# Kernel tuning notes

Hardware: AMD Instinct MI355X
Metric: run time of the kernel (lower is better)

## Reference

```python
import jax, jax.numpy as jnp
import numpy as np

N_NODES = 50000
N_EDGES = 800000
IN_C, HID_C, OUT_C = 256, 512, 256


def _linear_params(key, fan_in, fan_out):
    kw, kb = jax.random.split(key)
    bound = 1.0 / np.sqrt(fan_in)
    w = jax.random.uniform(kw, (fan_in, fan_out), jnp.float32, -bound, bound)
    b = jax.random.uniform(kb, (fan_out,), jnp.float32, -bound, bound)
    return w, b


def setup_inputs() -> dict:
    key = jax.random.key(0)
    ks = jax.random.split(key, 6)
    x = jax.random.normal(ks[0], (N_NODES, IN_C), jnp.float32)
    src = jax.random.randint(ks[1], (N_EDGES,), 0, N_NODES, jnp.int32)
    dst = jax.random.randint(ks[2], (N_EDGES,), 0, N_NODES, jnp.int32)
    w1, b1 = _linear_params(ks[3], IN_C, HID_C)
    w2, b2 = _linear_params(ks[4], HID_C, HID_C)
    w3, b3 = _linear_params(ks[5], HID_C, OUT_C)
    eps = jnp.zeros((), jnp.float32)  # GIN learnable eps, init 0
    return {"x": x, "src": src, "dst": dst,
            "w1": w1, "b1": b1, "eps1": eps,
            "w2": w2, "b2": b2, "eps2": eps,
            "w3": w3, "b3": b3, "eps3": eps}


def _gin_conv(h, src, dst, w, b, eps, n_nodes):
    # aggregate: (A @ h)[i] = sum over edges (src->dst==i) of h[src]
    agg = jax.ops.segment_sum(h[src], dst, num_segments=n_nodes)
    return ((1.0 + eps) * h + agg) @ w + b


def reference(x, src, dst, w1, b1, eps1, w2, b2, eps2, w3, b3, eps3):
    n = x.shape[0]
    # eval-mode forward: dropout is identity
    h = jax.nn.relu(_gin_conv(x, src, dst, w1, b1, eps1, n))
    h = jax.nn.relu(_gin_conv(h, src, dst, w2, b2, eps2, n))
    return _gin_conv(h, src, dst, w3, b3, eps3, n)
```

## Files before the change

### kernel.cpp

```cpp
#include <hip/hip_runtime.h>

#define N_NODES 50000
#define N_EDGES 800000
#define IN_C 256
#define HID_C 512
#define OUT_C 256
#define M_PAD 50048
#define NPASS 8
#define PASS_SHIFT 13

typedef unsigned short u16;
typedef unsigned int   u32;
typedef u16  u16x4 __attribute__((ext_vector_type(4)));
typedef u16  u16x8 __attribute__((ext_vector_type(8)));
typedef short s16x8 __attribute__((ext_vector_type(8)));
typedef float f32x4 __attribute__((ext_vector_type(4)));

__device__ __forceinline__ float bf2f(u16 h) {
    u32 u = ((u32)h) << 16;
    return __builtin_bit_cast(float, u);
}
__device__ __forceinline__ u16 f2bf(float f) {
    u32 u = __builtin_bit_cast(u32, f);
    u32 r = u + 0x7fffu + ((u >> 16) & 1u);
    return (u16)(r >> 16);
}
__device__ __forceinline__ void gload16(const void* g, void* l) {
    __builtin_amdgcn_global_load_lds(
        (const __attribute__((address_space(1))) u32*)g,
        (__attribute__((address_space(3))) u32*)l, 16, 0, 0);
}

__global__ void k_hist8(const int* __restrict__ src, const int* __restrict__ dst,
                        int* __restrict__ cnt8) {
    int e = blockIdx.x * 256 + threadIdx.x;
    if (e < N_EDGES) {
        int q = src[e] >> PASS_SHIFT;
        atomicAdd(&cnt8[dst[e] * NPASS + q], 1);
    }
}

__global__ void k_partial(const int* __restrict__ cnt, int* __restrict__ bsum, int total) {
    __shared__ int s[256];
    int i = blockIdx.x * 256 + threadIdx.x;
    int v = (i < total) ? cnt[i] : 0;
    s[threadIdx.x] = v; __syncthreads();
    for (int o = 128; o > 0; o >>= 1) {
        if (threadIdx.x < o) s[threadIdx.x] += s[threadIdx.x + o];
        __syncthreads();
    }
    if (threadIdx.x == 0) bsum[blockIdx.x] = s[0];
}

__global__ void k_scanb(int* __restrict__ bsum, int nb) {
    __shared__ int s[256];
    int carry = 0;
    for (int base = 0; base < nb; base += 256) {
        int i = base + threadIdx.x;
        int v = (i < nb) ? bsum[i] : 0;
        s[threadIdx.x] = v; __syncthreads();
        for (int o = 1; o < 256; o <<= 1) {
            int t = (threadIdx.x >= o) ? s[threadIdx.x - o] : 0;
            __syncthreads();
            s[threadIdx.x] += t;
            __syncthreads();
        }
        int tot = s[255];
        if (i < nb) bsum[i] = s[threadIdx.x] - v + carry;
        carry += tot;
        __syncthreads();
    }
}

__global__ void k_rowptr8(const int* __restrict__ cnt, const int* __restrict__ bsum,
                          int* __restrict__ rp, int* __restrict__ cur, int total) {
    __shared__ int s[256];
    int i = blockIdx.x * 256 + threadIdx.x;
    int v = (i < total) ? cnt[i] : 0;
    s[threadIdx.x] = v; __syncthreads();
    for (int o = 1; o < 256; o <<= 1) {
        int t = (threadIdx.x >= o) ? s[threadIdx.x - o] : 0;
        __syncthreads();
        s[threadIdx.x] += t;
        __syncthreads();
    }
    int excl = s[threadIdx.x] - v + bsum[blockIdx.x];
    if (i < total) { rp[i] = excl; cur[i] = excl; }
    if (i == total - 1) rp[total] = excl + v;
}

__global__ void k_scatter8(const int* __restrict__ src, const int* __restrict__ dst,
                           int* __restrict__ cur, int* __restrict__ col) {
    int e = blockIdx.x * 256 + threadIdx.x;
    if (e < N_EDGES) {
        int sv = src[e];
        int q = sv >> PASS_SHIFT;
        int p = atomicAdd(&cur[dst[e] * NPASS + q], 1);
        col[p] = sv;
    }
}

__global__ void k_wt(const float* __restrict__ w, u16* __restrict__ wt, int K, int N) {
    int idx = blockIdx.x * 256 + threadIdx.x;
    if (idx >= K * N) return;
    int n = idx / K, k = idx - n * K;
    wt[idx] = f2bf(w[(size_t)k * N + n]);
}

__global__ void k_x2bf(const float* __restrict__ x, u16* __restrict__ xb) {
    int i = blockIdx.x * 256 + threadIdx.x;
    if (i < N_NODES * IN_C / 4) {
        float4 v = ((const float4*)x)[i];
        u16x4 o;
        o[0] = f2bf(v.x); o[1] = f2bf(v.y); o[2] = f2bf(v.z); o[3] = f2bf(v.w);
        ((u16x4*)xb)[i] = o;
    }
}

template <int C, int EPI>
__global__ __launch_bounds__(256) void k_agg_stream(
    const u16* __restrict__ sm, const int* __restrict__ rp8,
    const int* __restrict__ col, const float* __restrict__ eps,
    const float* __restrict__ bias, void* __restrict__ out) {
    constexpr int NSLAB = C / 64;
    const int slab  = blockIdx.x & (NSLAB - 1);
    const int chunk = blockIdx.x / NSLAB;
    const int gid = threadIdx.x >> 4;
    const int ln  = threadIdx.x & 15;
    const int ch0 = slab * 64 + ln * 4;
    const int n = chunk * 16 + gid;
    if (n >= N_NODES) return;
    const float ep = 1.f + eps[0];

    const int rs = rp8[n * NPASS];
    const int re = rp8[n * NPASS + NPASS];
    float a0 = 0.f, a1 = 0.f, a2 = 0.f, a3 = 0.f;
    int e = rs;
    for (; e + 4 <= re; e += 4) {
        int s0 = col[e], s1 = col[e + 1], s2 = col[e + 2], s3 = col[e + 3];
        u16x4 v0 = *(const u16x4*)(sm + (size_t)s0 * C + ch0);
        u16x4 v1 = *(const u16x4*)(sm + (size_t)s1 * C + ch0);
        u16x4 v2 = *(const u16x4*)(sm + (size_t)s2 * C + ch0);
        u16x4 v3 = *(const u16x4*)(sm + (size_t)s3 * C + ch0);
        a0 += bf2f(v0[0]) + bf2f(v1[0]) + bf2f(v2[0]) + bf2f(v3[0]);
        a1 += bf2f(v0[1]) + bf2f(v1[1]) + bf2f(v2[1]) + bf2f(v3[1]);
        a2 += bf2f(v0[2]) + bf2f(v1[2]) + bf2f(v2[2]) + bf2f(v3[2]);
        a3 += bf2f(v0[3]) + bf2f(v1[3]) + bf2f(v2[3]) + bf2f(v3[3]);
    }
    for (; e < re; e++) {
        int s0 = col[e];
        u16x4 v0 = *(const u16x4*)(sm + (size_t)s0 * C + ch0);
        a0 += bf2f(v0[0]); a1 += bf2f(v0[1]); a2 += bf2f(v0[2]); a3 += bf2f(v0[3]);
    }

    u16x4 sv = *(const u16x4*)(sm + (size_t)n * C + ch0);
    float r0 = fmaf(ep, bf2f(sv[0]), a0);
    float r1 = fmaf(ep, bf2f(sv[1]), a1);
    float r2 = fmaf(ep, bf2f(sv[2]), a2);
    float r3 = fmaf(ep, bf2f(sv[3]), a3);
    if constexpr (EPI == 0) {
        u16x4 o;
        o[0] = f2bf(r0); o[1] = f2bf(r1); o[2] = f2bf(r2); o[3] = f2bf(r3);
        *(u16x4*)((u16*)out + (size_t)n * C + ch0) = o;
    } else {
        float4 bv = *(const float4*)(bias + ch0);
        float4 o;
        o.x = r0 + bv.x; o.y = r1 + bv.y; o.z = r2 + bv.z; o.w = r3 + bv.w;
        *(float4*)((float*)out + (size_t)n * C + ch0) = o;
    }
}

template <int K, int EPI>
__global__ __launch_bounds__(256, 2) void gemm_k(
    const u16* __restrict__ A, const u16* __restrict__ Wt,
    const float* __restrict__ bias, void* __restrict__ out,
    int N, int grid_n) {
    __shared__ u16 smem[16640];
    u16* Als = smem;
    u16* Bls = smem + 8192;
    const int tid  = threadIdx.x;
    const int wave = tid >> 6, lane = tid & 63;
    const int wm = wave >> 1, wn = wave & 1;
    const int bm = blockIdx.x / grid_n, bn = blockIdx.x % grid_n;
    const int m0 = bm * 128, n0 = bn * 128;
    const int sr = lane >> 3, sc = lane & 7;
    const int fr = lane & 15, kg = lane >> 4;

    f32x4 acc[4][4];
#pragma unroll
    for (int i = 0; i < 4; i++)
#pragma unroll
        for (int j = 0; j < 4; j++) acc[i][j] = (f32x4){0.f, 0.f, 0.f, 0.f};

    for (int kk = 0; kk < K; kk += 64) {
#pragma unroll
        for (int i = 0; i < 4; i++) {
            int rl = wave * 32 + i * 8 + sr;
            int cs = sc ^ (rl & 7);
            gload16(A  + (size_t)(m0 + rl) * K + kk + cs * 8,
                    &Als[(wave * 32 + i * 8) * 64]);
            gload16(Wt + (size_t)(n0 + rl) * K + kk + cs * 8,
                    &Bls[(wave * 32 + i * 8) * 64]);
        }
        asm volatile("s_waitcnt vmcnt(0)" ::: "memory");
        __syncthreads();

#pragma unroll
        for (int k2 = 0; k2 < 2; k2++) {
            s16x8 af[4], bfr[4];
#pragma unroll
            for (int mi = 0; mi < 4; mi++) {
                int r = wm * 64 + mi * 16 + fr;
                int c = (k2 * 4 + kg) ^ (r & 7);
                af[mi] = *(const s16x8*)&Als[r * 64 + c * 8];
            }
#pragma unroll
            for (int ni = 0; ni < 4; ni++) {
                int r = wn * 64 + ni * 16 + fr;
                int c = (k2 * 4 + kg) ^ (r & 7);
                bfr[ni] = *(const s16x8*)&Bls[r * 64 + c * 8];
            }
#pragma unroll
            for (int mi = 0; mi < 4; mi++)
#pragma unroll
                for (int ni = 0; ni < 4; ni++)
                    acc[mi][ni] = __builtin_amdgcn_mfma_f32_16x16x32_bf16(
                        af[mi], bfr[ni], acc[mi][ni], 0, 0, 0);
        }
        __syncthreads();
    }

    u16* Cls = smem;
#pragma unroll
    for (int ni = 0; ni < 4; ni++) {
        int c = wn * 64 + ni * 16 + fr;
        float bv = 0.f;
        if constexpr (EPI == 0) bv = bias[n0 + c];
#pragma unroll
        for (int mi = 0; mi < 4; mi++) {
#pragma unroll
            for (int j = 0; j < 4; j++) {
                int r = wm * 64 + mi * 16 + kg * 4 + j;
                float v = acc[mi][ni][j];
                if constexpr (EPI == 0) {
                    v += bv;
                    v = v > 0.f ? v : 0.f;
                }
                Cls[r * 130 + c] = f2bf(v);
            }
        }
    }
    __syncthreads();

    const int r2 = tid >> 1;
    const int cb = (tid & 1) * 64;
    if (m0 + r2 < N_NODES) {
        u16* orow = (u16*)out + (size_t)(m0 + r2) * N + n0 + cb;
#pragma unroll
        for (int k = 0; k < 8; k++) {
            u16x8 val = *(const u16x8*)&Cls[r2 * 130 + cb + k * 8];
            *(u16x8*)(orow + k * 8) = val;
        }
    }
}

extern "C" void kernel_launch(void* const* d_in, const int* in_sizes, int n_in,
                              void* d_out, int out_size, void* d_ws, size_t ws_size,
                              hipStream_t stream) {
    const float* x    = (const float*)d_in[0];
    const int*   src  = (const int*)d_in[1];
    const int*   dst  = (const int*)d_in[2];
    const float* w1   = (const float*)d_in[3];
    const float* b1   = (const float*)d_in[4];
    const float* eps1 = (const float*)d_in[5];
    const float* w2   = (const float*)d_in[6];
    const float* b2   = (const float*)d_in[7];
    const float* eps2 = (const float*)d_in[8];
    const float* w3   = (const float*)d_in[9];
    const float* b3   = (const float*)d_in[10];
    const float* eps3 = (const float*)d_in[11];

    char* ws = (char*)d_ws;
    size_t off = 0;
    auto take = [&](size_t bytes) {
        char* p = ws + off;
        off += (bytes + 255) & ~(size_t)255;
        return p;
    };
    const int TOT8 = N_NODES * NPASS;
    int* cnt8 = (int*)take((size_t)TOT8 * 4);
    int* rp8  = (int*)take((size_t)(TOT8 + 1) * 4);
    int* cur8 = (int*)take((size_t)TOT8 * 4);
    int* bsum = (int*)take(2048 * 4);
    int* col  = (int*)take((size_t)N_EDGES * 4);
    u16* w1t  = (u16*)take((size_t)IN_C * HID_C * 2);
    u16* w2t  = (u16*)take((size_t)HID_C * HID_C * 2);
    u16* w3t  = (u16*)take((size_t)HID_C * OUT_C * 2);
    u16* A0   = (u16*)take((size_t)M_PAD * IN_C * 2);
    u16* h1   = (u16*)take((size_t)M_PAD * HID_C * 2);
    u16* A1   = (u16*)take((size_t)M_PAD * HID_C * 2);
    u16* xb = A1;
    u16* h2 = h1;
    u16* g3 = A1;

    const int NB8 = (TOT8 + 255) / 256;
    const int NE  = (N_EDGES + 255) / 256;

    hipMemsetAsync(cnt8, 0, (size_t)TOT8 * 4, stream);
    k_hist8  <<<NE, 256, 0, stream>>>(src, dst, cnt8);
    k_partial<<<NB8, 256, 0, stream>>>(cnt8, bsum, TOT8);
    k_scanb  <<<1, 256, 0, stream>>>(bsum, NB8);
    k_rowptr8<<<NB8, 256, 0, stream>>>(cnt8, bsum, rp8, cur8, TOT8);
    k_scatter8<<<NE, 256, 0, stream>>>(src, dst, cur8, col);

    k_wt<<<(IN_C * HID_C + 255) / 256, 256, 0, stream>>>(w1, w1t, IN_C, HID_C);
    k_wt<<<(HID_C * HID_C + 255) / 256, 256, 0, stream>>>(w2, w2t, HID_C, HID_C);
    k_wt<<<(HID_C * OUT_C + 255) / 256, 256, 0, stream>>>(w3, w3t, HID_C, OUT_C);
    k_x2bf<<<(N_NODES * IN_C / 4 + 255) / 256, 256, 0, stream>>>(x, xb);

    const int NCH  = (N_NODES + 15) / 16;
    const int G512 = NCH * 8;
    const int G256 = NCH * 4;

    k_agg_stream<IN_C, 0><<<G256, 256, 0, stream>>>(xb, rp8, col, eps1, nullptr, A0);
    gemm_k<IN_C, 0><<<391 * (HID_C / 128), 256, 0, stream>>>(
        A0, w1t, b1, h1, HID_C, HID_C / 128);

    k_agg_stream<HID_C, 0><<<G512, 256, 0, stream>>>(h1, rp8, col, eps2, nullptr, A1);
    gemm_k<HID_C, 0><<<391 * (HID_C / 128), 256, 0, stream>>>(
        A1, w2t, b2, h2, HID_C, HID_C / 128);

    gemm_k<HID_C, 1><<<391 * (OUT_C / 128), 256, 0, stream>>>(
        h2, w3t, nullptr, g3, OUT_C, OUT_C / 128);
    k_agg_stream<OUT_C, 1><<<G256, 256, 0, stream>>>(g3, rp8, col, eps3, b3, (float*)d_out);
}
```

Before: 459.1 us.

## Sort nodes by degree for balanced aggregation and fuse prep kernels

Adds a counting sort of nodes by in-degree (histogram, scan, scatter) and has each aggregation thread group process nodes in that permuted order. Nodes with similar degree then share a wavefront, which is meant to cut divergence and idle lanes. The four weight-transpose and input-conversion launches are merged into one kernel to save launch overhead. The cost is three extra small kernels plus an indirection, and output rows are written in scattered rather than sequential order, which may hurt locality.

```diff
diff --git a/kernel.cpp b/kernel.cpp
--- a/kernel.cpp
+++ b/kernel.cpp
@@ -100,36 +100,83 @@
     }
 }
 
-__global__ void k_wt(const float* __restrict__ w, u16* __restrict__ wt, int K, int N) {
-    int idx = blockIdx.x * 256 + threadIdx.x;
+__global__ void k_deg(const int* __restrict__ rp8, int* __restrict__ dbin) {
+    int n = blockIdx.x * 256 + threadIdx.x;
+    if (n < N_NODES) {
+        int deg = rp8[n * NPASS + NPASS] - rp8[n * NPASS];
+        if (deg > 255) deg = 255;
+        atomicAdd(&dbin[deg], 1);
+    }
+}
+
+__global__ void k_degscan(const int* __restrict__ dbin, int* __restrict__ dcur) {
+    __shared__ int s[256];
+    int i = threadIdx.x;
+    int v = dbin[i];
+    s[i] = v; __syncthreads();
+    for (int o = 1; o < 256; o <<= 1) {
+        int t = (i >= o) ? s[i - o] : 0;
+        __syncthreads();
+        s[i] += t;
+        __syncthreads();
+    }
+    dcur[i] = s[i] - v;
+}
+
+__global__ void k_degscatter(const int* __restrict__ rp8, int* __restrict__ dcur,
+                             int* __restrict__ perm) {
+    int n = blockIdx.x * 256 + threadIdx.x;
+    if (n < N_NODES) {
+        int deg = rp8[n * NPASS + NPASS] - rp8[n * NPASS];
+        if (deg > 255) deg = 255;
+        int pos = atomicAdd(&dcur[deg], 1);
+        perm[pos] = n;
+    }
+}
+
+__device__ __forceinline__ void wt_body(const float* w, u16* wt, int K, int N, int idx) {
     if (idx >= K * N) return;
     int n = idx / K, k = idx - n * K;
     wt[idx] = f2bf(w[(size_t)k * N + n]);
 }
 
-__global__ void k_x2bf(const float* __restrict__ x, u16* __restrict__ xb) {
-    int i = blockIdx.x * 256 + threadIdx.x;
-    if (i < N_NODES * IN_C / 4) {
-        float4 v = ((const float4*)x)[i];
-        u16x4 o;
-        o[0] = f2bf(v.x); o[1] = f2bf(v.y); o[2] = f2bf(v.z); o[3] = f2bf(v.w);
-        ((u16x4*)xb)[i] = o;
+__global__ void k_prep(const float* __restrict__ w1, const float* __restrict__ w2,
+                       const float* __restrict__ w3, const float* __restrict__ x,
+                       u16* __restrict__ w1t, u16* __restrict__ w2t,
+                       u16* __restrict__ w3t, u16* __restrict__ xb) {
+    int b = blockIdx.x, t = threadIdx.x;
+    if (b < 512) {
+        wt_body(w1, w1t, IN_C, HID_C, b * 256 + t);
+    } else if (b < 1536) {
+        wt_body(w2, w2t, HID_C, HID_C, (b - 512) * 256 + t);
+    } else if (b < 2048) {
+        wt_body(w3, w3t, HID_C, OUT_C, (b - 1536) * 256 + t);
+    } else {
+        int i = (b - 2048) * 256 + t;
+        if (i < N_NODES * IN_C / 4) {
+            float4 v = ((const float4*)x)[i];
+            u16x4 o;
+            o[0] = f2bf(v.x); o[1] = f2bf(v.y); o[2] = f2bf(v.z); o[3] = f2bf(v.w);
+            ((u16x4*)xb)[i] = o;
+        }
     }
 }
 
 template <int C, int EPI>
 __global__ __launch_bounds__(256) void k_agg_stream(
     const u16* __restrict__ sm, const int* __restrict__ rp8,
-    const int* __restrict__ col, const float* __restrict__ eps,
-    const float* __restrict__ bias, void* __restrict__ out) {
+    const int* __restrict__ col, const int* __restrict__ perm,
+    const float* __restrict__ eps, const float* __restrict__ bias,
+    void* __restrict__ out) {
     constexpr int NSLAB = C / 64;
     const int slab  = blockIdx.x & (NSLAB - 1);
     const int chunk = blockIdx.x / NSLAB;
     const int gid = threadIdx.x >> 4;
     const int ln  = threadIdx.x & 15;
     const int ch0 = slab * 64 + ln * 4;
-    const int n = chunk * 16 + gid;
-    if (n >= N_NODES) return;
+    const int ni = chunk * 16 + gid;
+    if (ni >= N_NODES) return;
+    const int n = perm[ni];
     const float ep = 1.f + eps[0];
 
     const int rs = rp8[n * NPASS];
@@ -293,6 +340,9 @@
     int* cur8 = (int*)take((size_t)TOT8 * 4);
     int* bsum = (int*)take(2048 * 4);
     int* col  = (int*)take((size_t)N_EDGES * 4);
+    int* dbin = (int*)take(256 * 4);
+    int* dcur = (int*)take(256 * 4);
+    int* perm = (int*)take((size_t)N_NODES * 4);
     u16* w1t  = (u16*)take((size_t)IN_C * HID_C * 2);
     u16* w2t  = (u16*)take((size_t)HID_C * HID_C * 2);
     u16* w3t  = (u16*)take((size_t)HID_C * OUT_C * 2);
@@ -305,32 +355,38 @@
 
     const int NB8 = (TOT8 + 255) / 256;
     const int NE  = (N_EDGES + 255) / 256;
+    const int NBN = (N_NODES + 255) / 256;
 
     hipMemsetAsync(cnt8, 0, (size_t)TOT8 * 4, stream);
+    hipMemsetAsync(dbin, 0, 256 * 4, stream);
     k_hist8  <<<NE, 256, 0, stream>>>(src, dst, cnt8);
     k_partial<<<NB8, 256, 0, stream>>>(cnt8, bsum, TOT8);
     k_scanb  <<<1, 256, 0, stream>>>(bsum, NB8);
     k_rowptr8<<<NB8, 256, 0, stream>>>(cnt8, bsum, rp8, cur8, TOT8);
     k_scatter8<<<NE, 256, 0, stream>>>(src, dst, cur8, col);
 
-    k_wt<<<(IN_C * HID_C + 255) / 256, 256, 0, stream>>>(w1, w1t, IN_C, HID_C);
-    k_wt<<<(HID_C * HID_C + 255) / 256, 256, 0, stream>>>(w2, w2t, HID_C, HID_C);
-    k_wt<<<(HID_C * OUT_C + 255) / 256, 256, 0, stream>>>(w3, w3t, HID_C, OUT_C);
-    k_x2bf<<<(N_NODES * IN_C / 4 + 255) / 256, 256, 0, stream>>>(x, xb);
+    k_deg       <<<NBN, 256, 0, stream>>>(rp8, dbin);
+    k_degscan   <<<1, 256, 0, stream>>>(dbin, dcur);
+    k_degscatter<<<NBN, 256, 0, stream>>>(rp8, dcur, perm);
+
+    k_prep<<<2048 + 12500, 256, 0, stream>>>(w1, w2, w3, x, w1t, w2t, w3t, xb);
 
     const int NCH  = (N_NODES + 15) / 16;
     const int G512 = NCH * 8;
     const int G256 = NCH * 4;
 
-    k_agg_stream<IN_C, 0><<<G256, 256, 0, stream>>>(xb, rp8, col, eps1, nullptr, A0);
+    k_agg_stream<IN_C, 0><<<G256, 256, 0, stream>>>(
+        xb, rp8, col, perm, eps1, nullptr, A0);
     gemm_k<IN_C, 0><<<391 * (HID_C / 128), 256, 0, stream>>>(
         A0, w1t, b1, h1, HID_C, HID_C / 128);
 
-    k_agg_stream<HID_C, 0><<<G512, 256, 0, stream>>>(h1, rp8, col, eps2, nullptr, A1);
+    k_agg_stream<HID_C, 0><<<G512, 256, 0, stream>>>(
+        h1, rp8, col, perm, eps2, nullptr, A1);
     gemm_k<HID_C, 0><<<391 * (HID_C / 128), 256, 0, stream>>>(
         A1, w2t, b2, h2, HID_C, HID_C / 128);
 
     gemm_k<HID_C, 1><<<391 * (OUT_C / 128), 256, 0, stream>>>(
         h2, w3t, nullptr, g3, OUT_C, OUT_C / 128);
-    k_agg_stream<OUT_C, 1><<<G256, 256, 0, stream>>>(g3, rp8, col, eps3, b3, (float*)d_out);
-}
+    k_agg_stream<OUT_C, 1><<<G256, 256, 0, stream>>>(
+        g3, rp8, col, perm, eps3, b3, (float*)d_out);
+}
```

Measured after the change: 717.5 us. +56.3%, slower.
